# Kernel tuning notes

Hardware: AMD Instinct MI355X
Metric: run time of the kernel (lower is better)

The kernel has to match this reference:

```python
import jax, jax.numpy as jnp
import numpy as np
from jax import lax

KSIZE = 3
STRIDE = 1
RATE = 2
FUSE_K = 3
SCALE = 10.0
DN = ('NCHW', 'OIHW', 'NCHW')


def _same_pad_amount(size, k, s):
    out = (size + s - 1) // s
    pad = max(0, (out - 1) * s + k - size)
    return pad // 2, pad - pad // 2


def extract_patches(x, k, s):
    # torch.nn.Unfold with 'same' padding; returns [B, L, C, k, k], L row-major
    B, C, H, W = x.shape
    pt, pb = _same_pad_amount(H, k, s)
    pl, pr = _same_pad_amount(W, k, s)
    xp = jnp.pad(x, ((0, 0), (0, 0), (pt, pb), (pl, pr)))
    Ho = (H + s - 1) // s
    Wo = (W + s - 1) // s
    rows = (jnp.arange(Ho) * s)[:, None] + jnp.arange(k)[None, :]  # [Ho,k]
    cols = (jnp.arange(Wo) * s)[:, None] + jnp.arange(k)[None, :]  # [Wo,k]
    p = xp[:, :, rows, :][:, :, :, :, cols]  # [B,C,Ho,k,Wo,k]
    return p.transpose(0, 2, 4, 1, 3, 5).reshape(B, Ho * Wo, C, k, k)


def setup_inputs() -> dict:
    key = jax.random.key(0)
    kf, kb = jax.random.split(key)
    f = jax.random.normal(kf, (2, 128, 128, 128), dtype=jnp.float32)
    b = jax.random.normal(kb, (2, 128, 128, 128), dtype=jnp.float32)
    mask = jnp.zeros((1, 1, 128, 128), dtype=jnp.float32)  # all patches available
    return {"f": f, "b": b, "mask": mask}


def reference(f, b, mask):
    B, C, Hr, Wr = f.shape
    kernel = 2 * RATE
    # raw background patches for final aggregation: [B, Lb, C, 4, 4]
    raw_w = extract_patches(b, kernel, RATE * STRIDE)
    # nearest downsample by rate (src_idx = i*rate)
    f_ds = f[:, :, ::RATE, ::RATE]
    b_ds = b[:, :, ::RATE, ::RATE]
    Hf, Wf = f_ds.shape[2], f_ds.shape[3]
    Hb, Wb = b_ds.shape[2], b_ds.shape[3]
    L = Hb * Wb
    # matching patches: [B, L, C, 3, 3]
    w = extract_patches(b_ds, KSIZE, STRIDE)
    # mask patches (shared across batch, torch uses m[0])
    m_ds = mask[:, :, ::RATE, ::RATE]
    m = extract_patches(m_ds, KSIZE, STRIDE)[0]  # [L,1,3,3]
    mm = (jnp.mean(m, axis=(1, 2, 3)) == 0.0).astype(f.dtype).reshape(1, L, 1, 1)
    # L2-normalize patch filters (escape_NaN added elementwise before sum, as in torch)
    wn = w / jnp.sqrt(jnp.sum(w * w + 1e-4, axis=(2, 3, 4), keepdims=True))

    def score_one(xi, wi):
        # xi [C,Hf,Wf], wi [L,C,3,3] -> [L,Hf,Wf]
        return lax.conv_general_dilated(xi[None], wi, (1, 1), [(1, 1), (1, 1)],
                                        dimension_numbers=DN)[0]

    y = jax.vmap(score_one)(f_ds, wn)  # [B, L, Hf, Wf]

    # diagonal fuse: identity 3x3 conv on the [L, Hf*Wf] score matrix, twice with transpose
    fw = jnp.eye(FUSE_K, dtype=f.dtype).reshape(1, 1, FUSE_K, FUSE_K)

    def fuse_conv(t):
        return lax.conv_general_dilated(t, fw, (1, 1), [(1, 1), (1, 1)],
                                        dimension_numbers=DN)

    y = y.reshape(B, 1, Hb * Wb, Hf * Wf)
    y = fuse_conv(y).reshape(B, Hb, Wb, Hf, Wf)
    y = y.transpose(0, 2, 1, 4, 3).reshape(B, 1, L, Hf * Wf)
    y = fuse_conv(y).reshape(B, Wb, Hb, Wf, Hf)
    y = y.transpose(0, 2, 1, 4, 3).reshape(B, L, Hf, Wf)

    y = y * mm
    y = jax.nn.softmax(y * SCALE, axis=1) * mm

    def deconv_one(a, wc):
        # conv_transpose2d(a, wc, stride=rate, padding=1); wc [L,C,4,4]
        wt = jnp.flip(wc, (-2, -1)).transpose(1, 0, 2, 3)  # [C,L,4,4]
        pad = kernel - 1 - 1
        return lax.conv_general_dilated(a[None], wt, (1, 1), [(pad, pad), (pad, pad)],
                                        lhs_dilation=(RATE, RATE),
                                        dimension_numbers=DN)[0]

    out = jax.vmap(deconv_one)(y, raw_w) / 4.0  # [B, C, Hr, Wr]
    return out
```

## Files before the change

kernel.cpp:

```cpp
#include <hip/hip_runtime.h>
#include <cstdint>

typedef _Float16 f16x8 __attribute__((ext_vector_type(8)));
typedef float f32x4 __attribute__((ext_vector_type(4)));

typedef __attribute__((address_space(1))) void gvoid;
typedef __attribute__((address_space(3))) void lvoid;

__device__ __forceinline__ void gload16(const void* g, void* l) {
    __builtin_amdgcn_global_load_lds((gvoid*)g, (lvoid*)l, 16, 0, 0);
}

__device__ __forceinline__ void bar() {
    asm volatile("" ::: "memory");
    __builtin_amdgcn_s_barrier();
    asm volatile("" ::: "memory");
}
#define WAITV(N) asm volatile("s_waitcnt vmcnt(" #N ")" ::: "memory")
#define WAITL0 do { asm volatile("s_waitcnt lgkmcnt(0)" ::: "memory"); \
                    __builtin_amdgcn_sched_barrier(0); } while (0)

__global__ __launch_bounds__(256) void downsample_kernel(const float* __restrict__ f,
                                                         const float* __restrict__ b,
                                                         float* __restrict__ fds,
                                                         float* __restrict__ bds) {
    int idx = blockIdx.x * 256 + threadIdx.x;
    const float* src = blockIdx.y ? b : f;
    float* dst = blockIdx.y ? bds : fds;
    int bb = idx >> 19;
    int r = idx & 524287;
    int c = r >> 12, a = (r >> 6) & 63, v = r & 63;
    dst[idx] = src[(size_t)bb * 2097152 + (size_t)c * 16384 + (2 * a) * 128 + 2 * v];
}

__global__ __launch_bounds__(256) void build_mm_kernel(const float* __restrict__ mask,
                                                       float* __restrict__ mm) {
    int l = blockIdx.x * 256 + threadIdx.x;
    if (l >= 4096) return;
    int i = l >> 6, j = l & 63;
    float s = 0.f;
    #pragma unroll
    for (int dy = 0; dy < 3; ++dy)
        #pragma unroll
        for (int dx = 0; dx < 3; ++dx) {
            int a = i + dy - 1, b = j + dx - 1;
            if ((unsigned)a < 64u && (unsigned)b < 64u)
                s += mask[(2 * a) * 128 + 2 * b];
        }
    mm[l] = (s == 0.0f) ? 1.0f : 0.0f;
}

__global__ __launch_bounds__(256) void build_fpatch_kernel(const float* __restrict__ fds,
                                                           _Float16* __restrict__ Fp) {
    int bb = blockIdx.x >> 12;
    int p = blockIdx.x & 4095;
    const float* fb = fds + (size_t)bb * 524288;
    _Float16* Fpb = Fp + (size_t)bb * 4718592;
    int u = p >> 6, v = p & 63;
    for (int k = threadIdx.x; k < 1152; k += 256) {
        int c = k / 9;
        int s = k - 9 * c;
        int dy = s / 3, dx = s - 3 * dy;
        int a = u + dy - 1, bcol = v + dx - 1;
        float val = 0.f;
        if ((unsigned)a < 64u && (unsigned)bcol < 64u)
            val = fb[c * 4096 + a * 64 + bcol];
        Fpb[(size_t)p * 1152 + k] = (_Float16)val;
    }
}

__global__ __launch_bounds__(256) void build_wn_kernel(const float* __restrict__ bds,
                                                       _Float16* __restrict__ Wn) {
    __shared__ float wsh[1152];
    __shared__ float red[4];
    int bb = blockIdx.x >> 12;
    int l = blockIdx.x & 4095;
    const float* bp = bds + (size_t)bb * 524288;
    _Float16* Wnb = Wn + (size_t)bb * 4718592;
    int i = l >> 6, j = l & 63;
    float sq = 0.f;
    for (int k = threadIdx.x; k < 1152; k += 256) {
        int c = k / 9;
        int s = k - 9 * c;
        int dy = s / 3, dx = s - 3 * dy;
        int a = i + dy - 1, bcol = j + dx - 1;
        float val = 0.f;
        if ((unsigned)a < 64u && (unsigned)bcol < 64u)
            val = bp[c * 4096 + a * 64 + bcol];
        wsh[k] = val;
        sq += val * val;
    }
    #pragma unroll
    for (int off = 32; off > 0; off >>= 1) sq += __shfl_xor(sq, off);
    if ((threadIdx.x & 63) == 0) red[threadIdx.x >> 6] = sq;
    __syncthreads();
    float total = red[0] + red[1] + red[2] + red[3] + 0.1152f;
    float rinv = 1.0f / sqrtf(total);
    for (int k = threadIdx.x; k < 1152; k += 256)
        Wnb[(size_t)l * 1152 + k] = (_Float16)(wsh[k] * rinv);
}

__global__ __launch_bounds__(256) void build_vt_kernel(const float* __restrict__ b,
                                                       _Float16* __restrict__ Vt) {
    int bb = blockIdx.x >> 11;
    int n = blockIdx.x & 2047;
    const float* bp = b + (size_t)bb * 2097152;
    _Float16* Vtb = Vt + (size_t)bb * 8388608;
    int c = n >> 4, r = n & 15, rh = r >> 2, rw = r & 3;
    const float* bc = bp + (size_t)c * 16384;
    for (int l = threadIdx.x; l < 4096; l += 256) {
        int lh = l >> 6, lw = l & 63;
        int row = 2 * lh + rh - 1, col = 2 * lw + rw - 1;
        float val = 0.f;
        if ((unsigned)row < 128u && (unsigned)col < 128u)
            val = bc[row * 128 + col];
        Vtb[(size_t)n * 4096 + l] = (_Float16)val;
    }
}

template <int KSTR, int NTILES>
__device__ __forceinline__ void gemm_core(const _Float16* __restrict__ A,
                                          const _Float16* __restrict__ Bt,
                                          _Float16* __restrict__ C,
                                          _Float16* __restrict__ AsB,
                                          _Float16* __restrict__ BsB) {
    const int tid = threadIdx.x;
    const int lane = tid & 63;
    const int wave = tid >> 6;
    const int quad = lane >> 4;
    const int l16 = lane & 15;
    const int wm = wave >> 2;
    const int wn = wave & 3;
    const int bm = blockIdx.y * 256;
    const int bn = blockIdx.x * 256;

    f32x4 acc[8][4] = {};

    const int s0 = tid, s1 = 512 + tid;
    const int sr0 = s0 >> 2, sr1 = s1 >> 2;
    const int r0 = sr0 ^ ((sr0 >> 2) & 1);
    const int r1 = sr1 ^ ((sr1 >> 2) & 1);
    const int q0 = (s0 & 3) ^ (r0 & 3);
    const int q1 = (s1 & 3) ^ (r1 & 3);
    const int offA0 = (bm + r0) * KSTR + q0 * 8;
    const int offA1 = (bm + r1) * KSTR + q1 * 8;
    const int offB0 = (bn + r0) * KSTR + q0 * 8;
    const int offB1 = (bn + r1) * KSTR + q1 * 8;

#define STAGE_A(buf, kt, kh) do {                                                          \
        gload16(A + offA0 + (kt) * 64 + (kh) * 32, AsB + ((buf) * 2 + (kh)) * 8192 + tid * 8); \
        gload16(A + offA1 + (kt) * 64 + (kh) * 32, AsB + ((buf) * 2 + (kh)) * 8192 + 4096 + tid * 8); \
    } while (0)
#define STAGE_B(buf, kt, kh) do {                                                          \
        gload16(Bt + offB0 + (kt) * 64 + (kh) * 32, BsB + ((buf) * 2 + (kh)) * 8192 + tid * 8); \
        gload16(Bt + offB1 + (kt) * 64 + (kh) * 32, BsB + ((buf) * 2 + (kh)) * 8192 + 4096 + tid * 8); \
    } while (0)

    const int c2 = (l16 >> 2) & 1;
    const int rdoff = ((l16 ^ c2) * 32) + ((quad ^ (l16 & 3)) * 8);

    f16x8 afr[4], bfr[4];
    auto LDA = [&](int buf, int kh, int mh) {
        #pragma unroll
        for (int mi = 0; mi < 4; ++mi)
            afr[mi] = *(const f16x8*)&AsB[((buf) * 2 + (kh)) * 8192 +
                                          (wm * 128 + ((mh) * 4 + mi) * 16) * 32 + rdoff];
    };
    auto LDB = [&](int buf, int kh) {
        #pragma unroll
        for (int ni = 0; ni < 4; ++ni)
            bfr[ni] = *(const f16x8*)&BsB[((buf) * 2 + (kh)) * 8192 +
                                          (wn * 64 + ni * 16) * 32 + rdoff];
    };
    auto MM = [&](int mh) {
        __builtin_amdgcn_s_setprio(1);
        #pragma unroll
        for (int mi = 0; mi < 4; ++mi)
            #pragma unroll
            for (int ni = 0; ni < 4; ++ni)
                acc[mh * 4 + mi][ni] = __builtin_amdgcn_mfma_f32_16x16x32_f16(
                    afr[mi], bfr[ni], acc[mh * 4 + mi][ni], 0, 0, 0);
        __builtin_amdgcn_s_setprio(0);
    };

    STAGE_A(0, 0, 0); STAGE_B(0, 0, 0);
    STAGE_A(0, 0, 1); STAGE_B(0, 0, 1);
    STAGE_A(1, 1, 0); STAGE_B(1, 1, 0);
    WAITV(4);
    bar();

    #pragma unroll 1
    for (int i = 0; i < NTILES / 2 - 1; ++i) {
        const int t0 = 2 * i;
        LDA(0, 0, 0); LDB(0, 0); STAGE_A(1, t0 + 1, 1);
        bar(); WAITL0; MM(0); bar();
        LDA(0, 0, 1); STAGE_B(1, t0 + 1, 1);
        bar(); WAITL0; MM(1); bar();
        LDA(0, 1, 0); LDB(0, 1); STAGE_A(0, t0 + 2, 0);
        bar(); WAITL0; MM(0); bar();
        LDA(0, 1, 1); STAGE_B(0, t0 + 2, 0); WAITV(4);
        bar(); WAITL0; MM(1); bar();
        LDA(1, 0, 0); LDB(1, 0); STAGE_A(0, t0 + 2, 1);
        bar(); WAITL0; MM(0); bar();
        LDA(1, 0, 1); STAGE_B(0, t0 + 2, 1);
        bar(); WAITL0; MM(1); bar();
        LDA(1, 1, 0); LDB(1, 1); STAGE_A(1, t0 + 3, 0);
        bar(); WAITL0; MM(0); bar();
        LDA(1, 1, 1); STAGE_B(1, t0 + 3, 0); WAITV(4);
        bar(); WAITL0; MM(1); bar();
    }

    LDA(0, 0, 0); LDB(0, 0); STAGE_A(1, NTILES - 1, 1);
    bar(); WAITL0; MM(0); bar();
    LDA(0, 0, 1); STAGE_B(1, NTILES - 1, 1);
    bar(); WAITL0; MM(1); bar();
    LDA(0, 1, 0); LDB(0, 1);
    bar(); WAITL0; MM(0); bar();
    LDA(0, 1, 1);
    bar(); WAITL0; MM(1); WAITV(0); bar();
    LDA(1, 0, 0); LDB(1, 0); bar(); WAITL0; MM(0); bar();
    LDA(1, 0, 1);            bar(); WAITL0; MM(1); bar();
    LDA(1, 1, 0); LDB(1, 1); bar(); WAITL0; MM(0); bar();
    LDA(1, 1, 1);            bar(); WAITL0; MM(1);

#undef STAGE_A
#undef STAGE_B

    #pragma unroll
    for (int mi = 0; mi < 8; ++mi)
        #pragma unroll
        for (int ni = 0; ni < 4; ++ni)
            #pragma unroll
            for (int r = 0; r < 4; ++r) {
                int row = bm + wm * 128 + mi * 16 + quad * 4 + r;
                int col = bn + wn * 64 + ni * 16 + l16;
                C[(size_t)row * 4096 + col] = (_Float16)acc[mi][ni][r];
            }
}

__global__ __launch_bounds__(512, 2) void gemm1_kernel(const _Float16* __restrict__ Fp,
                                                       const _Float16* __restrict__ Wn,
                                                       _Float16* __restrict__ S0) {
    __shared__ __align__(16) _Float16 As[2][2][8192];
    __shared__ __align__(16) _Float16 Bs[2][2][8192];
    const int z = blockIdx.z;
    gemm_core<1152, 18>(Fp + (size_t)z * 4718592, Wn + (size_t)z * 4718592,
                        S0 + (size_t)z * 16777216, &As[0][0][0], &Bs[0][0][0]);
}

__global__ __launch_bounds__(512, 2) void gemm2_kernel(const _Float16* __restrict__ Vt,
                                                       const _Float16* __restrict__ att0,
                                                       const _Float16* __restrict__ att1,
                                                       _Float16* __restrict__ OTh) {
    __shared__ __align__(16) _Float16 As[2][2][8192];
    __shared__ __align__(16) _Float16 Bs[2][2][8192];
    const int z = blockIdx.z;
    gemm_core<4096, 64>(Vt + (size_t)z * 8388608, z ? att1 : att0,
                        OTh + (size_t)z * 8388608, &As[0][0][0], &Bs[0][0][0]);
}

__global__ __launch_bounds__(256) void fuse_softmax_kernel(const _Float16* __restrict__ S0,
                                                           const float* __restrict__ mm,
                                                           _Float16* __restrict__ att0,
                                                           _Float16* __restrict__ att1) {
    __shared__ float red[4];
    const int tid = threadIdx.x;
    const int lane = tid & 63;
    const int wave = tid >> 6;
    int g = blockIdx.x;
    int p_global = ((g & 7) << 10) | (g >> 3);
    const int bb = p_global >> 12;
    const int p = p_global & 4095;
    const _Float16* S = S0 + (size_t)bb * 16777216;
    _Float16* att = bb ? att1 : att0;
    const int pbase = ((p & 63) << 6) | (p >> 6);

    float acc[16];
    #pragma unroll
    for (int k = 0; k < 16; ++k) acc[k] = 0.f;

    #pragma unroll
    for (int t2 = -1; t2 <= 1; ++t2) {
        int b2 = pbase + t2;
        if ((unsigned)b2 >= 4096u) continue;
        int pp = ((b2 & 63) << 6) | (b2 >> 6);
        #pragma unroll
        for (int t1 = -1; t1 <= 1; ++t1) {
            int rr = pp + t1;
            if ((unsigned)rr >= 4096u) continue;
            const _Float16* row = S + (size_t)rr * 4096;
            #pragma unroll
            for (int k = 0; k < 16; ++k) {
                int l = k * 256 + tid;
                int i = (k * 256 + wave * 64) >> 6;
                int it2 = i + t2;
                if (it2 >= 0 && it2 < 64) {
                    int c = l + t2 * 64 + t1;
                    if ((unsigned)c < 4096u)
                        acc[k] += (float)row[c];
                } else if (it2 == 64) {
                    if (lane <= 62) {
                        int c = lane + 1 + t1;
                        if ((unsigned)c < 4096u) acc[k] += (float)row[c];
                    }
                } else {
                    if (lane >= 1) {
                        int c = 4031 + lane + t1;
                        if ((unsigned)c < 4096u) acc[k] += (float)row[c];
                    }
                }
            }
        }
    }

    float mv[16];
    float lmax = -1e30f;
    #pragma unroll
    for (int k = 0; k < 16; ++k) {
        int l = k * 256 + tid;
        mv[k] = mm[l];
        float lg = acc[k] * mv[k] * 10.0f;
        acc[k] = lg;
        lmax = fmaxf(lmax, lg);
    }
    #pragma unroll
    for (int off = 32; off > 0; off >>= 1) lmax = fmaxf(lmax, __shfl_xor(lmax, off));
    if (lane == 0) red[wave] = lmax;
    __syncthreads();
    lmax = fmaxf(fmaxf(red[0], red[1]), fmaxf(red[2], red[3]));
    __syncthreads();

    float lsum = 0.f;
    #pragma unroll
    for (int k = 0; k < 16; ++k) {
        float e = __expf(acc[k] - lmax);
        acc[k] = e;
        lsum += e;
    }
    #pragma unroll
    for (int off = 32; off > 0; off >>= 1) lsum += __shfl_xor(lsum, off);
    if (lane == 0) red[wave] = lsum;
    __syncthreads();
    float inv = 1.0f / (red[0] + red[1] + red[2] + red[3]);
    #pragma unroll
    for (int k = 0; k < 16; ++k) {
        int l = k * 256 + tid;
        att[(size_t)p * 4096 + l] = (_Float16)(acc[k] * inv * mv[k]);
    }
}

__global__ __launch_bounds__(256) void assemble_kernel(const _Float16* __restrict__ OTh,
                                                       float* __restrict__ out) {
    int idx = blockIdx.x * 256 + threadIdx.x;
    int bb = idx >> 21;
    int w = idx & 2097151;
    const _Float16* OTb = OTh + (size_t)bb * 8388608;
    int x = w & 127, y = (w >> 7) & 127, c = w >> 14;
    int r0 = (y + 1) & 1, s0 = (x + 1) & 1;
    float acc = 0.f;
    #pragma unroll
    for (int a = 0; a < 2; ++a) {
        int rh = r0 + 2 * a;
        int ph = (y + 1 - rh) >> 1;
        if ((unsigned)ph < 64u) {
            #pragma unroll
            for (int bq = 0; bq < 2; ++bq) {
                int rw = s0 + 2 * bq;
                int pw = (x + 1 - rw) >> 1;
                if ((unsigned)pw < 64u)
                    acc += (float)OTb[(size_t)(c * 16 + rh * 4 + rw) * 4096 + ph * 64 + pw];
            }
        }
    }
    out[idx] = 0.25f * acc;
}

extern "C" void kernel_launch(void* const* d_in, const int* in_sizes, int n_in,
                              void* d_out, int out_size, void* d_ws, size_t ws_size,
                              hipStream_t stream) {
    const float* f = (const float*)d_in[0];
    const float* b = (const float*)d_in[1];
    const float* mask = (const float*)d_in[2];
    float* out = (float*)d_out;
    char* ws = (char*)d_ws;

    float* mm = (float*)ws;
    _Float16* Fp = (_Float16*)(ws + 16384);
    _Float16* Wn = (_Float16*)(ws + 16384 + 18874368);
    _Float16* att0 = (_Float16*)(ws + 16384);
    _Float16* S0 = (_Float16*)(ws + 37765120);
    _Float16* Vt = (_Float16*)(ws + 37765120);
    _Float16* OTh = (_Float16*)(ws + 37765120 + 33554432);
    float* fds = (float*)(ws + 104873984);
    float* bds = (float*)(ws + 104873984 + 4194304);
    _Float16* att1 = (_Float16*)(ws + 104873984);

    downsample_kernel<<<dim3(4096, 2), 256, 0, stream>>>(f, b, fds, bds);
    build_mm_kernel<<<16, 256, 0, stream>>>(mask, mm);
    build_fpatch_kernel<<<8192, 256, 0, stream>>>(fds, Fp);
    build_wn_kernel<<<8192, 256, 0, stream>>>(bds, Wn);

    gemm1_kernel<<<dim3(16, 16, 2), 512, 0, stream>>>(Fp, Wn, S0);
    fuse_softmax_kernel<<<8192, 256, 0, stream>>>(S0, mm, att0, att1);

    build_vt_kernel<<<4096, 256, 0, stream>>>(b, Vt);
    gemm2_kernel<<<dim3(16, 8, 2), 512, 0, stream>>>(Vt, att0, att1, OTh);
    assemble_kernel<<<16384, 256, 0, stream>>>(OTh, out);
}
```

Measured before the change: 433.2 us.

## Vectorize fuse-softmax row loads/stores and drop explicit LDS waits in GEMM

```diff
diff --git a/kernel.cpp b/kernel.cpp
--- a/kernel.cpp
+++ b/kernel.cpp
@@ -17,8 +17,6 @@
     asm volatile("" ::: "memory");
 }
 #define WAITV(N) asm volatile("s_waitcnt vmcnt(" #N ")" ::: "memory")
-#define WAITL0 do { asm volatile("s_waitcnt lgkmcnt(0)" ::: "memory"); \
-                    __builtin_amdgcn_sched_barrier(0); } while (0)
 
 __global__ __launch_bounds__(256) void downsample_kernel(const float* __restrict__ f,
                                                          const float* __restrict__ b,
@@ -193,35 +191,35 @@
     for (int i = 0; i < NTILES / 2 - 1; ++i) {
         const int t0 = 2 * i;
         LDA(0, 0, 0); LDB(0, 0); STAGE_A(1, t0 + 1, 1);
-        bar(); WAITL0; MM(0); bar();
+        bar(); MM(0); bar();
         LDA(0, 0, 1); STAGE_B(1, t0 + 1, 1);
-        bar(); WAITL0; MM(1); bar();
+        bar(); MM(1); bar();
         LDA(0, 1, 0); LDB(0, 1); STAGE_A(0, t0 + 2, 0);
-        bar(); WAITL0; MM(0); bar();
+        bar(); MM(0); bar();
         LDA(0, 1, 1); STAGE_B(0, t0 + 2, 0); WAITV(4);
-        bar(); WAITL0; MM(1); bar();
+        bar(); MM(1); bar();
         LDA(1, 0, 0); LDB(1, 0); STAGE_A(0, t0 + 2, 1);
-        bar(); WAITL0; MM(0); bar();
+        bar(); MM(0); bar();
         LDA(1, 0, 1); STAGE_B(0, t0 + 2, 1);
-        bar(); WAITL0; MM(1); bar();
+        bar(); MM(1); bar();
         LDA(1, 1, 0); LDB(1, 1); STAGE_A(1, t0 + 3, 0);
-        bar(); WAITL0; MM(0); bar();
+        bar(); MM(0); bar();
         LDA(1, 1, 1); STAGE_B(1, t0 + 3, 0); WAITV(4);
-        bar(); WAITL0; MM(1); bar();
+        bar(); MM(1); bar();
     }
 
     LDA(0, 0, 0); LDB(0, 0); STAGE_A(1, NTILES - 1, 1);
-    bar(); WAITL0; MM(0); bar();
+    bar(); MM(0); bar();
     LDA(0, 0, 1); STAGE_B(1, NTILES - 1, 1);
-    bar(); WAITL0; MM(1); bar();
+    bar(); MM(1); bar();
     LDA(0, 1, 0); LDB(0, 1);
-    bar(); WAITL0; MM(0); bar();
+    bar(); MM(0); bar();
     LDA(0, 1, 1);
-    bar(); WAITL0; MM(1); WAITV(0); bar();
-    LDA(1, 0, 0); LDB(1, 0); bar(); WAITL0; MM(0); bar();
-    LDA(1, 0, 1);            bar(); WAITL0; MM(1); bar();
-    LDA(1, 1, 0); LDB(1, 1); bar(); WAITL0; MM(0); bar();
-    LDA(1, 1, 1);            bar(); WAITL0; MM(1);
+    bar(); MM(1); WAITV(0); bar();
+    LDA(1, 0, 0); LDB(1, 0); bar(); MM(0); bar();
+    LDA(1, 0, 1);            bar(); MM(1); bar();
+    LDA(1, 1, 0); LDB(1, 1); bar(); MM(0); bar();
+    LDA(1, 1, 1);            bar(); MM(1);
 
 #undef STAGE_A
 #undef STAGE_B
@@ -275,40 +273,47 @@
     _Float16* att = bb ? att1 : att0;
     const int pbase = ((p & 63) << 6) | (p >> 6);
 
+    const int i  = tid >> 2;
+    const int j0 = (tid & 3) << 4;
+    const int l0 = tid * 16;
+
     float acc[16];
     #pragma unroll
-    for (int k = 0; k < 16; ++k) acc[k] = 0.f;
+    for (int e = 0; e < 16; ++e) acc[e] = 0.f;
 
     #pragma unroll
     for (int t2 = -1; t2 <= 1; ++t2) {
         int b2 = pbase + t2;
         if ((unsigned)b2 >= 4096u) continue;
         int pp = ((b2 & 63) << 6) | (b2 >> 6);
+        const int it2 = i + t2;
         #pragma unroll
         for (int t1 = -1; t1 <= 1; ++t1) {
             int rr = pp + t1;
             if ((unsigned)rr >= 4096u) continue;
             const _Float16* row = S + (size_t)rr * 4096;
-            #pragma unroll
-            for (int k = 0; k < 16; ++k) {
-                int l = k * 256 + tid;
-                int i = (k * 256 + wave * 64) >> 6;
-                int it2 = i + t2;
-                if (it2 >= 0 && it2 < 64) {
-                    int c = l + t2 * 64 + t1;
-                    if ((unsigned)c < 4096u)
-                        acc[k] += (float)row[c];
-                } else if (it2 == 64) {
-                    if (lane <= 62) {
-                        int c = lane + 1 + t1;
-                        if ((unsigned)c < 4096u) acc[k] += (float)row[c];
-                    }
-                } else {
-                    if (lane >= 1) {
-                        int c = 4031 + lane + t1;
-                        if ((unsigned)c < 4096u) acc[k] += (float)row[c];
-                    }
+            if ((unsigned)it2 < 64u) {
+                const int ws = it2 * 64 + j0 - 1;
+                float w[18];
+                f16x8 v0 = *(const f16x8*)&row[ws + 1];
+                f16x8 v1 = *(const f16x8*)&row[ws + 9];
+                w[0]  = (ws >= 0) ? (float)row[ws] : 0.f;
+                #pragma unroll
+                for (int x = 0; x < 8; ++x) {
+                    w[1 + x] = (float)v0[x];
+                    w[9 + x] = (float)v1[x];
                 }
+                w[17] = (ws + 17 < 4096) ? (float)row[ws + 17] : 0.f;
+                #pragma unroll
+                for (int e = 0; e < 16; ++e) acc[e] += w[e + 1 + t1];
+            } else if (it2 == 64) {
+                #pragma unroll
+                for (int e = 0; e < 16; ++e)
+                    if (j0 + e <= 62) acc[e] += (float)row[j0 + e + 1 + t1];
+            } else {
+                #pragma unroll
+                for (int e = 0; e < 16; ++e)
+                    if (j0 + e >= 1) acc[e] += (float)row[4031 + j0 + e + t1];
             }
         }
     }
@@ -316,11 +321,10 @@
     float mv[16];
     float lmax = -1e30f;
     #pragma unroll
-    for (int k = 0; k < 16; ++k) {
-        int l = k * 256 + tid;
-        mv[k] = mm[l];
-        float lg = acc[k] * mv[k] * 10.0f;
-        acc[k] = lg;
+    for (int e = 0; e < 16; ++e) {
+        mv[e] = mm[l0 + e];
+        float lg = acc[e] * mv[e] * 10.0f;
+        acc[e] = lg;
         lmax = fmaxf(lmax, lg);
     }
     #pragma unroll
@@ -332,21 +336,23 @@
 
     float lsum = 0.f;
     #pragma unroll
-    for (int k = 0; k < 16; ++k) {
-        float e = __expf(acc[k] - lmax);
-        acc[k] = e;
-        lsum += e;
+    for (int e = 0; e < 16; ++e) {
+        float ex = __expf(acc[e] - lmax);
+        acc[e] = ex;
+        lsum += ex;
     }
     #pragma unroll
     for (int off = 32; off > 0; off >>= 1) lsum += __shfl_xor(lsum, off);
     if (lane == 0) red[wave] = lsum;
     __syncthreads();
     float inv = 1.0f / (red[0] + red[1] + red[2] + red[3]);
-    #pragma unroll
-    for (int k = 0; k < 16; ++k) {
-        int l = k * 256 + tid;
-        att[(size_t)p * 4096 + l] = (_Float16)(acc[k] * inv * mv[k]);
-    }
+
+    _Float16 outv[16];
+    #pragma unroll
+    for (int e = 0; e < 16; ++e) outv[e] = (_Float16)(acc[e] * inv * mv[e]);
+    _Float16* dst = att + (size_t)p * 4096 + l0;
+    *(f16x8*)&dst[0] = *(const f16x8*)&outv[0];
+    *(f16x8*)&dst[8] = *(const f16x8*)&outv[8];
 }
 
 __global__ __launch_bounds__(256) void assemble_kernel(const _Float16* __restrict__ OTh,
```

Result: no change. 433.3 us (median of 2 runs) (+0.0%).
